# Performance work log

Measured on AMD Instinct MI355X. Metric: run time of the kernel, lower is better.

The kernel has to match this reference:

```python
import jax, jax.numpy as jnp
import numpy as np

B, C, OC, H, W = 2, 64, 128, 96, 96
HD, DI, N, R, K = C // 2, C, 16, 2, 4  # VSSBlock: hidden=C/2, d_inner=2*hidden=C, d_state, dt_rank, 4 scan dirs
EPS = 1e-5


def _conv(x, w, b, pad, groups=1):
    y = jax.lax.conv_general_dilated(x, w, (1, 1), pad, feature_group_count=groups,
                                     dimension_numbers=('NCHW', 'OIHW', 'NCHW'))
    return y + b[None, :, None, None]


def _ln(x, w, b):
    m = x.mean(-1, keepdims=True)
    v = x.var(-1, keepdims=True)
    return (x - m) * jax.lax.rsqrt(v + EPS) * w + b


def _selective_scan(xs, dts, Bs, Cs, A, D):
    # xs, dts: (B,K,DI,L); Bs, Cs: (B,K,N,L); A: (K,DI,N); D: (K,DI)
    dts = jax.nn.softplus(dts)

    def step(h, inp):
        u_t, dt_t, B_t, C_t = inp
        dA = jnp.exp(dt_t[..., None] * A)                         # (B,K,DI,N)
        h = dA * h + (dt_t * u_t)[..., None] * B_t[:, :, None, :]
        return h, jnp.einsum('bkdn,bkn->bkd', h, C_t)

    seq = (jnp.moveaxis(xs, -1, 0), jnp.moveaxis(dts, -1, 0),
           jnp.moveaxis(Bs, -1, 0), jnp.moveaxis(Cs, -1, 0))
    h0 = jnp.zeros(xs.shape[:3] + (A.shape[-1],), xs.dtype)
    _, ys = jax.lax.scan(step, h0, seq)
    return jnp.moveaxis(ys, 0, -1) + D[None, :, :, None] * xs


def _vss_block(x, ln_w, ln_b, in_w, conv_w, conv_b, xproj_w, dtproj_w, dtproj_b,
               A_logs, Ds, on_w, on_b, out_w):
    # x: (B,H,W,HD); VMamba SS2D with 4-direction cross-scan + residual
    b, hh, ww, _ = x.shape
    L = hh * ww
    h = _ln(x, ln_w, ln_b)
    xz = h @ in_w                                   # (B,H,W,2*DI)
    xp, z = jnp.split(xz, 2, axis=-1)
    xc = jnp.transpose(xp, (0, 3, 1, 2))            # (B,DI,H,W)
    xc = jax.nn.silu(_conv(xc, conv_w, conv_b, ((1, 1), (1, 1)), groups=DI))
    x_flat = xc.reshape(b, DI, L)
    x_wh = jnp.transpose(xc, (0, 1, 3, 2)).reshape(b, DI, L)
    x2 = jnp.stack([x_flat, x_wh], axis=1)
    xs = jnp.concatenate([x2, jnp.flip(x2, -1)], axis=1)      # (B,4,DI,L)
    x_dbl = jnp.einsum('bkdl,kcd->bkcl', xs, xproj_w)
    dts, Bs, Cs = jnp.split(x_dbl, [R, R + N], axis=2)
    dts = jnp.einsum('bkrl,kdr->bkdl', dts, dtproj_w) + dtproj_b[None, :, :, None]
    A = -jnp.exp(A_logs)
    ys = _selective_scan(xs, dts, Bs, Cs, A, Ds)              # (B,4,DI,L)
    inv = jnp.flip(ys[:, 2:4], -1)
    unwh = lambda t: jnp.transpose(t.reshape(b, DI, ww, hh), (0, 1, 3, 2)).reshape(b, DI, L)
    y = ys[:, 0] + inv[:, 0] + unwh(ys[:, 1]) + unwh(inv[:, 1])
    y = jnp.transpose(y.reshape(b, DI, hh, ww), (0, 2, 3, 1))
    y = _ln(y, on_w, on_b) * jax.nn.silu(z)
    return x + y @ out_w


def _forward(x, ms_dw33_w, ms_dw33_b, ms_in_w, ms_in_b, ms_scale,
             vss_ln_w, vss_ln_b, vss_in_w, vss_conv_w, vss_conv_b, vss_xproj_w,
             vss_dtproj_w, vss_dtproj_b, vss_A_logs, vss_Ds, vss_on_w, vss_on_b, vss_out_w,
             ma_conv_w, ma_conv_b, adw_h_w, adw_h_b, adw_w_w, adw_w_b,
             pw_w, pw_b, bn_w, bn_b, bn_mean, bn_var):
    vss = (vss_ln_w, vss_ln_b, vss_in_w, vss_conv_w, vss_conv_b, vss_xproj_w,
           vss_dtproj_w, vss_dtproj_b, vss_A_logs, vss_Ds, vss_on_w, vss_on_b, vss_out_w)
    # --- MambaSplit (shared VSSBlock applied to both channel halves) ---
    xd = _conv(x, ms_dw33_w, ms_dw33_b, ((1, 1), (1, 1)), groups=C)
    x1, x2 = jnp.split(xd, 2, axis=1)

    def branch(xp):
        y = _vss_block(jnp.transpose(xp, (0, 2, 3, 1)), *vss)
        return ms_scale * xp + jnp.transpose(y, (0, 3, 1, 2))

    xm = jnp.concatenate([branch(x1), branch(x2)], axis=1)
    m = xm.mean((2, 3), keepdims=True)
    v = xm.var((2, 3), keepdims=True)
    xm = (xm - m) * jax.lax.rsqrt(v + EPS) * ms_in_w[None, :, None, None] + ms_in_b[None, :, None, None]
    xm = jax.nn.leaky_relu(xm, 0.01)
    # --- MaxAvg (global avg+max pool -> 3x3 conv on 1x1 map -> sigmoid gate) ---
    pooled = jnp.concatenate([x.mean((2, 3), keepdims=True), x.max((2, 3), keepdims=True)], axis=1)
    gate = jax.nn.sigmoid(_conv(pooled, ma_conv_w, ma_conv_b, ((1, 1), (1, 1))))
    xs_ = xm + gate * x
    # --- AxialDW ---
    xs_ = xs_ + _conv(xs_, adw_h_w, adw_h_b, ((1, 1), (0, 0)), groups=C) \
              + _conv(xs_, adw_w_w, adw_w_b, ((0, 0), (1, 1)), groups=C)
    # --- BN (eval) + ReLU, 1x1 conv, 2x2 maxpool ---
    skip = jax.nn.relu((xs_ - bn_mean[None, :, None, None]) * jax.lax.rsqrt(bn_var[None, :, None, None] + EPS)
                       * bn_w[None, :, None, None] + bn_b[None, :, None, None])
    out = _conv(skip, pw_w, pw_b, ((0, 0), (0, 0)))
    down = jax.lax.reduce_window(out, -jnp.inf, jax.lax.max, (1, 1, 2, 2), (1, 1, 2, 2), 'VALID')
    return down, skip


def setup_inputs() -> dict:
    key = jax.random.key(0)
    ks = jax.random.split(key, 16)
    r = lambda i, shape, s=0.02: jax.random.normal(ks[i], shape, jnp.float32) * s
    return {
        'x': jax.random.normal(ks[0], (B, C, H, W), jnp.float32),
        'ms_dw33_w': r(1, (C, 1, 3, 3), 0.1), 'ms_dw33_b': jnp.zeros(C),
        'ms_in_w': jnp.ones(C), 'ms_in_b': jnp.zeros(C),
        'ms_scale': jnp.ones((1,)),
        'vss_ln_w': jnp.ones(HD), 'vss_ln_b': jnp.zeros(HD),
        'vss_in_w': r(2, (HD, 2 * DI)),
        'vss_conv_w': r(3, (DI, 1, 3, 3), 0.1), 'vss_conv_b': jnp.zeros(DI),
        'vss_xproj_w': r(4, (K, R + 2 * N, DI)),
        'vss_dtproj_w': r(5, (K, DI, R), 0.1), 'vss_dtproj_b': r(6, (K, DI), 0.1),
        'vss_A_logs': jnp.tile(jnp.log(jnp.arange(1, N + 1, dtype=jnp.float32)), (K, DI, 1)),
        'vss_Ds': jnp.ones((K, DI)),
        'vss_on_w': jnp.ones(DI), 'vss_on_b': jnp.zeros(DI),
        'vss_out_w': r(7, (DI, HD)),
        'ma_conv_w': r(8, (C, 2 * C, 3, 3), 0.05), 'ma_conv_b': jnp.zeros(C),
        'adw_h_w': r(9, (C, 1, 3, 1), 0.1), 'adw_h_b': jnp.zeros(C),
        'adw_w_w': r(10, (C, 1, 1, 3), 0.1), 'adw_w_b': jnp.zeros(C),
        'pw_w': r(11, (OC, C, 1, 1)), 'pw_b': jnp.zeros(OC),
        'bn_w': jnp.ones(C), 'bn_b': jnp.zeros(C),
        'bn_mean': jnp.zeros(C), 'bn_var': jnp.ones(C),
    }


def reference(x, ms_dw33_w, ms_dw33_b, ms_in_w, ms_in_b, ms_scale,
              vss_ln_w, vss_ln_b, vss_in_w, vss_conv_w, vss_conv_b, vss_xproj_w,
              vss_dtproj_w, vss_dtproj_b, vss_A_logs, vss_Ds, vss_on_w, vss_on_b, vss_out_w,
              ma_conv_w, ma_conv_b, adw_h_w, adw_h_b, adw_w_w, adw_w_b,
              pw_w, pw_b, bn_w, bn_b, bn_mean, bn_var):
    return _forward(x, ms_dw33_w, ms_dw33_b, ms_in_w, ms_in_b, ms_scale,
                    vss_ln_w, vss_ln_b, vss_in_w, vss_conv_w, vss_conv_b, vss_xproj_w,
                    vss_dtproj_w, vss_dtproj_b, vss_A_logs, vss_Ds, vss_on_w, vss_on_b, vss_out_w,
                    ma_conv_w, ma_conv_b, adw_h_w, adw_h_b, adw_w_w, adw_w_b,
                    pw_w, pw_b, bn_w, bn_b, bn_mean, bn_var)
```

## Files before the change

kernel.cpp:

```cpp
#include <hip/hip_runtime.h>
#include <hip/hip_bf16.h>

typedef __hip_bfloat16 bf16;
#define DEV __device__ __forceinline__

constexpr int B_ = 2, C_ = 64, H_ = 96, W_ = 96, L_ = 9216;
constexpr int HD_ = 32, DI_ = 64, N_ = 16, K_ = 4, BB_ = 4;
constexpr int OC_ = 128;
constexpr int CH_ = 384, CL_ = 24;
constexpr int SEGN = 32, SEGC = 12;
constexpr int BROW = 20;
constexpr float EPSF = 1e-5f;
constexpr int DOWN_SZ = B_ * OC_ * 48 * 48;

typedef __attribute__((ext_vector_type(8))) short short8;
typedef __attribute__((ext_vector_type(4))) float f32x4;
typedef __attribute__((ext_vector_type(2))) float f32x2;

DEV float softplusf(float x) { return x > 15.f ? x : __logf(1.f + __expf(x)); }
DEV float b2f(bf16 v) { return __bfloat162float(v); }
DEV float lo16f(unsigned v) { return __uint_as_float(v << 16); }
DEV float hi16f(unsigned v) { return __uint_as_float(v & 0xffff0000u); }
DEV f32x2 pk2(unsigned w) { f32x2 r = {lo16f(w), hi16f(w)}; return r; }
DEV void unpk8(uint4 a, float* v) {
  v[0] = lo16f(a.x); v[1] = hi16f(a.x); v[2] = lo16f(a.y); v[3] = hi16f(a.y);
  v[4] = lo16f(a.z); v[5] = hi16f(a.z); v[6] = lo16f(a.w); v[7] = hi16f(a.w);
}
DEV void unpk(uint4 a, uint4 b, float* v) {
  unpk8(a, v); unpk8(b, v + 8);
}

__constant__ float kLogN[16] = {
  0.0f, 0.69314718f, 1.09861229f, 1.38629436f, 1.60943791f, 1.79175947f,
  1.94591015f, 2.07944154f, 2.19722458f, 2.30258509f, 2.39789527f,
  2.48490665f, 2.56494936f, 2.63905733f, 2.70805020f, 2.77258872f};

DEV void pow_tree2(float e1, f32x2* ep) {
  float e2 = e1 * e1;
  ep[0].x = e1; ep[0].y = e2;
  f32x2 b2v = {e2, e2};
  ep[1] = ep[0] * b2v;
  float e4 = ep[1].y;
  f32x2 b4v = {e4, e4};
  ep[2] = ep[0] * b4v;
  ep[3] = ep[1] * b4v;
  float e8 = ep[3].y;
  f32x2 b8v = {e8, e8};
  ep[4] = ep[0] * b8v;
  ep[5] = ep[1] * b8v;
  ep[6] = ep[2] * b8v;
  ep[7] = ep[3] * b8v;
}

__global__ __launch_bounds__(256, 4) void k_front(
    const float* __restrict__ x, const float* __restrict__ dw33w,
    const float* __restrict__ dw33b, const float* __restrict__ lnw,
    const float* __restrict__ lnb, const float* __restrict__ inw,
    const float* __restrict__ xpw, const float* __restrict__ alog,
    float* __restrict__ xd, bf16* __restrict__ xzAh, bf16* __restrict__ xzBh,
    bf16* __restrict__ wh, float* __restrict__ aux) {
  int bb = blockIdx.y, t = threadIdx.x;
  int b = bb & 1, co = (bb >> 1) * HD_;
  int idx0 = blockIdx.x * 32;
  if (bb == 0) {
    int i = blockIdx.x * 256 + t;
    if (i < 144 * 64) {
      int n = i >> 6;
      wh[i] = __float2bfloat16(n < 136 ? xpw[i] : 0.f);
    }
    if (blockIdx.x == 0) {
      int kd = t;
      const float* al = alog + kd * N_;
      float a0 = al[0];
      bool lin = true;
#pragma unroll
      for (int n = 1; n < N_; n++) lin = lin && (fabsf(al[n] - a0 - kLogN[n]) < 3e-5f);
      aux[kd] = -__expf(a0);
      aux[256 + kd] = lin ? 1.f : 0.f;
#pragma unroll
      for (int n = 0; n < N_; n++) aux[512 + kd * N_ + n] = -__expf(al[n]);
    }
  }
  __shared__ float xds[32 * 36];
  __shared__ float meanA[32], rstdA[32];
  for (int i = t; i < 1024; i += 256) {
    int cl = i >> 5, ii = i & 31;
    int sp = idx0 + ii, wi = sp % 96, hi = sp / 96;
    int cg = b * C_ + co + cl;
    float acc = dw33b[co + cl];
#pragma unroll
    for (int dy = -1; dy <= 1; dy++) {
      int hh = hi + dy; if (hh < 0 || hh >= H_) continue;
#pragma unroll
      for (int dx = -1; dx <= 1; dx++) {
        int ww = wi + dx; if (ww < 0 || ww >= W_) continue;
        acc = fmaf(x[(size_t)cg * L_ + sp + dy * 96 + dx],
                   dw33w[(co + cl) * 9 + (dy + 1) * 3 + (dx + 1)], acc);
      }
    }
    xds[cl * 36 + ii] = acc;
    xd[(size_t)cg * L_ + sp] = acc;
  }
  __syncthreads();
  if (t < 32) {
    float s = 0.f, sq = 0.f;
#pragma unroll
    for (int c = 0; c < 32; c++) { float v = xds[c * 36 + t]; s += v; sq = fmaf(v, v, sq); }
    float mean = s * (1.f / HD_);
    float var = sq * (1.f / HD_) - mean * mean;
    meanA[t] = mean; rstdA[t] = rsqrtf(var + EPSF);
  }
  __syncthreads();
  for (int i = t; i < 1024; i += 256) {
    int c = i >> 5, idx = i & 31;
    float v = xds[c * 36 + idx];
    xds[c * 36 + idx] = (v - meanA[idx]) * rstdA[idx] * lnw[c] + lnb[c];
  }
  __syncthreads();
  int oc = t & 127, g = t >> 7;
  float acc[16];
#pragma unroll
  for (int j = 0; j < 16; j++) acc[j] = 0.f;
  for (int c = 0; c < 32; c++) {
    float wv = inw[c * 128 + oc];
    const float4* row = reinterpret_cast<const float4*>(&xds[c * 36 + g * 16]);
#pragma unroll
    for (int j4 = 0; j4 < 4; j4++) {
      float4 xv = row[j4];
      acc[j4 * 4 + 0] = fmaf(xv.x, wv, acc[j4 * 4 + 0]);
      acc[j4 * 4 + 1] = fmaf(xv.y, wv, acc[j4 * 4 + 1]);
      acc[j4 * 4 + 2] = fmaf(xv.z, wv, acc[j4 * 4 + 2]);
      acc[j4 * 4 + 3] = fmaf(xv.w, wv, acc[j4 * 4 + 3]);
    }
  }
  int occ = oc & 63;
  if (oc < 64) {
#pragma unroll
    for (int j = 0; j < 16; j++)
      xzAh[(size_t)(bb * L_ + idx0 + g * 16 + j) * 64 + occ] = __float2bfloat16(acc[j]);
  } else {
#pragma unroll
    for (int j = 0; j < 16; j++)
      xzBh[(size_t)(bb * L_ + idx0 + g * 16 + j) * 64 + occ] = __float2bfloat16(acc[j]);
  }
}

__global__ void k_dwsilu(const bf16* __restrict__ xzAh, const float* __restrict__ cw,
                         const float* __restrict__ cb, bf16* __restrict__ xch,
                         bf16* __restrict__ xcht) {
  int t = blockIdx.x * 256 + threadIdx.x;
  int d = t & 63, idx = (t >> 6) % L_, bb = t / (L_ * DI_);
  int wi = idx % W_, hi = idx / W_;
  float acc = cb[d];
#pragma unroll
  for (int dy = -1; dy <= 1; dy++) {
    int hh = hi + dy; if (hh < 0 || hh >= H_) continue;
#pragma unroll
    for (int dx = -1; dx <= 1; dx++) {
      int ww = wi + dx; if (ww < 0 || ww >= W_) continue;
      acc = fmaf(b2f(xzAh[(size_t)(bb * L_ + hh * W_ + ww) * 64 + d]),
                 cw[d * 9 + (dy + 1) * 3 + (dx + 1)], acc);
    }
  }
  acc = acc / (1.f + __expf(-acc));
  bf16 v = __float2bfloat16(acc);
  xch[t] = v;
  int idx_t = wi * 96 + hi;
  xcht[((size_t)bb * L_ + idx_t) * DI_ + d] = v;
}

__global__ __launch_bounds__(256, 4) void k_xdbl_mfma(
    const bf16* __restrict__ xch, const bf16* __restrict__ wh,
    float* __restrict__ xdblB, float* __restrict__ xdblC) {
  int w = threadIdx.x >> 6, lane = threadIdx.x & 63;
  int bb = blockIdx.y;
  int mtile = blockIdx.x * 4 + w;
  int idx0 = mtile * 16;
  int m = lane & 15, quad = lane >> 4;
  const bf16* arow = xch + ((size_t)bb * L_ + idx0 + m) * 64 + quad * 8;
  short8 a0 = *reinterpret_cast<const short8*>(arow);
  short8 a1 = *reinterpret_cast<const short8*>(arow + 32);
  int ntb = blockIdx.z * 3;
#pragma unroll
  for (int it = 0; it < 3; it++) {
    int nt = ntb + it;
    int n = nt * 16 + m;
    const bf16* brow = wh + n * 64 + quad * 8;
    short8 b0 = *reinterpret_cast<const short8*>(brow);
    short8 b1 = *reinterpret_cast<const short8*>(brow + 32);
    f32x4 acc = {0.f, 0.f, 0.f, 0.f};
    acc = __builtin_amdgcn_mfma_f32_16x16x32_bf16(a0, b0, acc, 0, 0, 0);
    acc = __builtin_amdgcn_mfma_f32_16x16x32_bf16(a1, b1, acc, 0, 0, 0);
    if (n < 136) {
      int k4 = (n >= 102) ? 3 : (n >= 68) ? 2 : (n >= 34) ? 1 : 0;
      int c = n - k4 * 34;
#pragma unroll
      for (int i = 0; i < 4; i++) {
        int r = idx0 + quad * 4 + i;
        int hi2 = r / 96, wi2 = r - hi2 * 96;
        int tr = wi2 * 96 + hi2;
        int ls = (k4 == 0) ? r : (k4 == 1) ? tr : (k4 == 2) ? (L_ - 1 - r) : (L_ - 1 - tr);
        size_t row = (size_t)(bb * K_ + k4) * L_ + ls;
        if (c < 2)       xdblB[row * BROW + 16 + c] = acc[i];
        else if (c < 18) xdblB[row * BROW + (c - 2)] = acc[i];
        else             xdblC[row * 16 + (c - 18)] = acc[i];
      }
    }
  }
}

__global__ __launch_bounds__(256, 4) void k_scan1(
    const float* __restrict__ xdblB, const bf16* __restrict__ xch,
    const bf16* __restrict__ xcht, const float* __restrict__ dtw,
    const float* __restrict__ dtb, const float* __restrict__ aux,
    bf16* __restrict__ hbuf, float* __restrict__ ssum) {
  int w = threadIdx.x >> 6, d = threadIdx.x & 63;
  int bx = blockIdx.x;
  int chunk = bx * 4 + w, k = blockIdx.y, bb = blockIdx.z;
  const float* bB = xdblB + (size_t)(bb * K_ + k) * L_ * BROW;
  __shared__ __align__(16) float sB[96 * BROW];
  {
    const uint4* src = (const uint4*)(bB + (size_t)bx * 96 * BROW);
    uint4* dst = (uint4*)sB;
    for (int i = threadIdx.x; i < 480; i += 256) dst[i] = src[i];
  }
  __syncthreads();
  float w0 = dtw[(k * DI_ + d) * 2 + 0], w1 = dtw[(k * DI_ + d) * 2 + 1];
  float bia = dtb[k * DI_ + d];
  float A1 = aux[k * 64 + d];
  bool chain = (__ballot(aux[256 + k * 64 + d] > 0.5f) == ~0ull);
  const bf16* ub = ((k & 1) ? xcht : xch) + (size_t)bb * L_ * DI_;
  int ls0 = chunk * CL_;
  int uidx0 = (k & 2) ? (L_ - 1 - ls0) : ls0;
  int ustep = (k & 2) ? -1 : 1;
  float S = 0.f;
  size_t base = (size_t)((bb * K_ + k) * CH_ + chunk) * DI_ + d;
  if (chain) {
    float uv[CL_];
    const bf16* up = ub + (size_t)uidx0 * DI_ + d;
#pragma unroll
    for (int s = 0; s < CL_; s++) uv[s] = b2f(up[s * ustep * DI_]);
    f32x2 h2[8];
#pragma unroll
    for (int i = 0; i < 8; i++) { h2[i].x = 0.f; h2[i].y = 0.f; }
#pragma unroll
    for (int s = 0; s < CL_; s++) {
      const float* p = sB + (w * CL_ + s) * BROW;
      float dt = softplusf(fmaf(p[16], w0, fmaf(p[17], w1, bia)));
      S += dt;
      float du = dt * uv[s];
      f32x2 du2 = {du, du};
      f32x2 ep2[8];
      pow_tree2(__expf(dt * A1), ep2);
#pragma unroll
      for (int i = 0; i < 8; i++)
        h2[i] = ep2[i] * h2[i] + du2 * (*(const f32x2*)(p + 2 * i));
    }
#pragma unroll
    for (int i = 0; i < 8; i++) {
      hbuf[base * N_ + 2 * i]     = __float2bfloat16(h2[i].x);
      hbuf[base * N_ + 2 * i + 1] = __float2bfloat16(h2[i].y);
    }
  } else {
    float h[N_];
#pragma unroll
    for (int n = 0; n < N_; n++) h[n] = 0.f;
    float A[N_];
#pragma unroll
    for (int n = 0; n < N_; n++) A[n] = aux[512 + (k * 64 + d) * N_ + n];
    for (int s = 0; s < CL_; s++) {
      const float* p = sB + (w * CL_ + s) * BROW;
      float u = b2f(ub[(size_t)(uidx0 + s * ustep) * DI_ + d]);
      float dt = softplusf(fmaf(p[16], w0, fmaf(p[17], w1, bia)));
      S += dt;
      float du = dt * u;
#pragma unroll
      for (int n = 0; n < N_; n++) h[n] = fmaf(__expf(dt * A[n]), h[n], du * p[n]);
    }
#pragma unroll
    for (int n = 0; n < N_; n++) hbuf[base * N_ + n] = __float2bfloat16(h[n]);
  }
  ssum[base] = S;
}

__global__ __launch_bounds__(256, 4) void k_scan2a(
    const float* __restrict__ aux, const float* __restrict__ ssum,
    bf16* __restrict__ hbuf, float* __restrict__ cumS,
    float* __restrict__ segH, float* __restrict__ segS) {
  int t = blockIdx.x * 256 + threadIdx.x;
  int n = t & 15, d = (t >> 4) & 63, kk = (t >> 10) & 3, bb = (t >> 12) & 3, seg = t >> 14;
  float A = aux[512 + (kk * 64 + d) * N_ + n];
  size_t row = (size_t)(bb * K_ + kk) * CH_ * DI_ + d;
  float hp = 0.f, Sc = 0.f;
#pragma unroll 4
  for (int j = 0; j < SEGC; j++) {
    int c = seg * SEGC + j;
    size_t sb = row + (size_t)c * DI_;
    float S = ssum[sb];
    float hl = b2f(hbuf[sb * N_ + n]);
    hbuf[sb * N_ + n] = __float2bfloat16(hp);
    if (n == 0) cumS[sb] = Sc;
    hp = fmaf(__expf(A * S), hp, hl);
    Sc += S;
  }
  size_t sbase = (size_t)(bb * K_ + kk) * SEGN + seg;
  segH[(sbase * DI_ + d) * N_ + n] = hp;
  if (n == 0) segS[sbase * DI_ + d] = Sc;
}

__global__ void k_scan2b(const float* __restrict__ aux, float* __restrict__ segH,
                         const float* __restrict__ segS) {
  int t = blockIdx.x * 256 + threadIdx.x;
  int n = t & 15, d = (t >> 4) & 63, kk = (t >> 10) & 3, bb = t >> 12;
  float A = aux[512 + (kk * 64 + d) * N_ + n];
  float hp = 0.f;
  for (int seg = 0; seg < SEGN; seg++) {
    size_t sbase = (size_t)(bb * K_ + kk) * SEGN + seg;
    size_t si = (sbase * DI_ + d) * N_ + n;
    float H = segH[si];
    float E = __expf(A * segS[sbase * DI_ + d]);
    segH[si] = hp;
    hp = fmaf(E, hp, H);
  }
}

__global__ __launch_bounds__(256, 4) void k_scan3(
    const float* __restrict__ xdblB, const float* __restrict__ xdblC,
    const bf16* __restrict__ xch, const bf16* __restrict__ xcht,
    const float* __restrict__ dtw, const float* __restrict__ dtb,
    const float* __restrict__ Dsw, const float* __restrict__ aux,
    const bf16* __restrict__ hbuf, const float* __restrict__ cumS,
    const float* __restrict__ segH, bf16* __restrict__ ydir) {
  int w = threadIdx.x >> 6, d = threadIdx.x & 63;
  int bx = blockIdx.x;
  int chunk = bx * 4 + w, k = blockIdx.y, bb = blockIdx.z;
  const float* bB = xdblB + (size_t)(bb * K_ + k) * L_ * BROW;
  const float* bC = xdblC + (size_t)(bb * K_ + k) * L_ * 16;
  __shared__ __align__(16) float sB[96 * BROW];
  __shared__ __align__(16) float sC[96 * 16];
  {
    const uint4* srcB = (const uint4*)(bB + (size_t)bx * 96 * BROW);
    uint4* dstB = (uint4*)sB;
    for (int i = threadIdx.x; i < 480; i += 256) dstB[i] = srcB[i];
    const uint4* srcC = (const uint4*)(bC + (size_t)bx * 96 * 16);
    uint4* dstC = (uint4*)sC;
    for (int i = threadIdx.x; i < 384; i += 256) dstC[i] = srcC[i];
  }
  __syncthreads();
  float w0 = dtw[(k * DI_ + d) * 2 + 0], w1 = dtw[(k * DI_ + d) * 2 + 1];
  float bia = dtb[k * DI_ + d];
  float Dk = Dsw[k * DI_ + d];
  float A1 = aux[k * 64 + d];
  bool chain = (__ballot(aux[256 + k * 64 + d] > 0.5f) == ~0ull);
  size_t base = (size_t)((bb * K_ + k) * CH_ + chunk) * DI_ + d;
  int seg = chunk / SEGC;
  size_t sbase = (size_t)(bb * K_ + k) * SEGN + seg;
  float Sc = cumS[base];
  const bf16* ub = ((k & 1) ? xcht : xch) + (size_t)bb * L_ * DI_;
  bf16* yb = ydir + (size_t)(bb * K_ + k) * L_ * DI_;
  int ls0 = chunk * CL_;
  int uidx0 = (k & 2) ? (L_ - 1 - ls0) : ls0;
  int ustep = (k & 2) ? -1 : 1;
  const bf16* hb = hbuf + base * N_;
  const float* Hin = segH + (sbase * DI_ + d) * N_;
  if (chain) {
    float uv[CL_];
    const bf16* up = ub + (size_t)uidx0 * DI_ + d;
#pragma unroll
    for (int s = 0; s < CL_; s++) uv[s] = b2f(up[s * ustep * DI_]);
    f32x2 h2[8];
    {
      uint4 qh0 = *(const uint4*)hb, qh1 = *(const uint4*)(hb + 8);
      h2[0] = pk2(qh0.x); h2[1] = pk2(qh0.y); h2[2] = pk2(qh0.z); h2[3] = pk2(qh0.w);
      h2[4] = pk2(qh1.x); h2[5] = pk2(qh1.y); h2[6] = pk2(qh1.z); h2[7] = pk2(qh1.w);
      f32x2 ep2[8];
      pow_tree2(__expf(A1 * Sc), ep2);
#pragma unroll
      for (int i = 0; i < 8; i++)
        h2[i] = ep2[i] * (*(const f32x2*)(Hin + 2 * i)) + h2[i];
    }
#pragma unroll
    for (int s = 0; s < CL_; s++) {
      int lr = w * CL_ + s;
      const float* p = sB + lr * BROW;
      const float* pc = sC + lr * 16;
      float dt = softplusf(fmaf(p[16], w0, fmaf(p[17], w1, bia)));
      float du = dt * uv[s];
      f32x2 du2 = {du, du};
      f32x2 ep2[8];
      pow_tree2(__expf(dt * A1), ep2);
      f32x2 y2 = {0.f, 0.f};
#pragma unroll
      for (int i = 0; i < 8; i++) {
        h2[i] = ep2[i] * h2[i] + du2 * (*(const f32x2*)(p + 2 * i));
        y2 = h2[i] * (*(const f32x2*)(pc + 2 * i)) + y2;
      }
      float y = fmaf(Dk, uv[s], y2.x + y2.y);
      yb[(size_t)(ls0 + s) * DI_ + d] = __float2bfloat16(y);
    }
  } else {
    float h[N_];
    {
      uint4 qh0 = *(const uint4*)hb, qh1 = *(const uint4*)(hb + 8);
      unpk(qh0, qh1, h);
#pragma unroll
      for (int n = 0; n < N_; n++) {
        float A = aux[512 + (k * 64 + d) * N_ + n];
        h[n] = fmaf(__expf(A * Sc), Hin[n], h[n]);
      }
    }
    float A[N_];
#pragma unroll
    for (int n = 0; n < N_; n++) A[n] = aux[512 + (k * 64 + d) * N_ + n];
    for (int s = 0; s < CL_; s++) {
      int lr = w * CL_ + s;
      const float* p = sB + lr * BROW;
      const float* pc = sC + lr * 16;
      float u = b2f(ub[(size_t)(uidx0 + s * ustep) * DI_ + d]);
      float dt = softplusf(fmaf(p[16], w0, fmaf(p[17], w1, bia)));
      float du = dt * u;
      float y = 0.f;
#pragma unroll
      for (int n = 0; n < N_; n++) {
        h[n] = fmaf(__expf(dt * A[n]), h[n], du * p[n]);
        y = fmaf(h[n], pc[n], y);
      }
      y = fmaf(Dk, u, y);
      yb[(size_t)(ls0 + s) * DI_ + d] = __float2bfloat16(y);
    }
  }
}

__global__ void k_combine(const bf16* __restrict__ ydir, const bf16* __restrict__ xzBh,
                          const float* __restrict__ xd, const float* __restrict__ onw,
                          const float* __restrict__ onb, const float* __restrict__ outw,
                          const float* __restrict__ mssc, float* __restrict__ xm) {
  int w = threadIdx.x >> 6, d = threadIdx.x & 63;
  int idx = blockIdx.x * 4 + w, bb = blockIdx.y;
  int b = bb & 1, co = (bb >> 1) * HD_;
  int hii = idx / 96, wii = idx - hii * 96;
  int lt = wii * 96 + hii;
  const bf16* yd = ydir + (size_t)bb * K_ * L_ * DI_;
  float y = b2f(yd[((size_t)0 * L_ + idx) * DI_ + d])
          + b2f(yd[((size_t)1 * L_ + lt) * DI_ + d])
          + b2f(yd[((size_t)2 * L_ + (L_ - 1 - idx)) * DI_ + d])
          + b2f(yd[((size_t)3 * L_ + (L_ - 1 - lt)) * DI_ + d]);
  float s = y, sq = y * y;
#pragma unroll
  for (int m = 1; m < 64; m <<= 1) { s += __shfl_xor(s, m, 64); sq += __shfl_xor(sq, m, 64); }
  float mean = s * (1.f / DI_);
  float var = sq * (1.f / DI_) - mean * mean;
  float rstd = rsqrtf(var + EPSF);
  float yn = (y - mean) * rstd * onw[d] + onb[d];
  float z = b2f(xzBh[(size_t)(bb * L_ + idx) * 64 + d]);
  float g = yn * (z / (1.f + __expf(-z)));
  __shared__ float gs[4][DI_];
  gs[w][d] = g;
  __syncthreads();
  if (d < HD_) {
    float acc = 0.f;
#pragma unroll
    for (int dd = 0; dd < DI_; dd++) acc = fmaf(gs[w][dd], outw[dd * HD_ + d], acc);
    size_t xi = (size_t)(b * C_ + co + d) * L_ + idx;
    float xp = xd[xi];
    xm[xi] = mssc[0] * xp + xp + acc;
  }
}

__global__ __launch_bounds__(1024) void k_stats(
    const float* __restrict__ xm, const float* __restrict__ x,
    float* __restrict__ inm, float* __restrict__ inr,
    float* __restrict__ xmean, float* __restrict__ xmax) {
  int bc = blockIdx.x, t = threadIdx.x;
  const float* pm = xm + (size_t)bc * L_;
  const float* px = x + (size_t)bc * L_;
  float s = 0.f, sq = 0.f, xs = 0.f, mx = -1e30f;
  for (int i = t; i < L_; i += 1024) {
    float v = pm[i]; s += v; sq = fmaf(v, v, sq);
    float xv = px[i]; xs += xv; mx = fmaxf(mx, xv);
  }
  __shared__ float red[64];
#pragma unroll
  for (int m = 1; m < 64; m <<= 1) {
    s += __shfl_xor(s, m, 64); sq += __shfl_xor(sq, m, 64);
    xs += __shfl_xor(xs, m, 64); mx = fmaxf(mx, __shfl_xor(mx, m, 64));
  }
  int wid = t >> 6;
  if ((t & 63) == 0) { red[wid] = s; red[16 + wid] = sq; red[32 + wid] = xs; red[48 + wid] = mx; }
  __syncthreads();
  if (t == 0) {
    s = 0.f; sq = 0.f; xs = 0.f; mx = -1e30f;
#pragma unroll
    for (int i = 0; i < 16; i++) {
      s += red[i]; sq += red[16 + i]; xs += red[32 + i]; mx = fmaxf(mx, red[48 + i]);
    }
    float mean = s * (1.f / L_);
    float var = sq * (1.f / L_) - mean * mean;
    inm[bc] = mean;
    inr[bc] = rsqrtf(var + EPSF);
    xmean[bc] = xs * (1.f / L_);
    xmax[bc] = mx;
  }
}

__global__ void k_axbn(const float* __restrict__ xm, const float* __restrict__ x,
                       const float* __restrict__ inm, const float* __restrict__ inr,
                       const float* __restrict__ msw, const float* __restrict__ msb,
                       const float* __restrict__ xmean, const float* __restrict__ xmax,
                       const float* __restrict__ maw, const float* __restrict__ mab,
                       const float* __restrict__ hw, const float* __restrict__ hb,
                       const float* __restrict__ wwt, const float* __restrict__ wb,
                       const float* __restrict__ bnw, const float* __restrict__ bnb,
                       const float* __restrict__ bnm, const float* __restrict__ bnv,
                       float* __restrict__ skipo) {
  constexpr int NEL = B_ * C_ * L_;
  int t0 = blockIdx.x * 256;
  int t = t0 + threadIdx.x;
  int bc = t0 / L_, c = bc & 63, b = bc >> 6;
  __shared__ float gsh;
  __shared__ float sxs[448];
  if (threadIdx.x < 64) {
    int ic = threadIdx.x;
    float p = xmean[b * 64 + ic] * maw[(c * 128 + ic) * 9 + 4]
            + xmax[b * 64 + ic] * maw[(c * 128 + 64 + ic) * 9 + 4];
#pragma unroll
    for (int m = 1; m < 64; m <<= 1) p += __shfl_xor(p, m, 64);
    if (ic == 0) gsh = 1.f / (1.f + __expf(-(p + mab[c])));
  }
  __syncthreads();
  float gate = gsh, im = inm[bc], ir = inr[bc], mw = msw[c], mb = msb[c];
  for (int i = threadIdx.x; i < 448; i += 256) {
    int tt = t0 - 96 + i;
    tt = tt < 0 ? 0 : (tt >= NEL ? NEL - 1 : tt);
    float v = xm[tt];
    v = (v - im) * ir * mw + mb;
    v = v > 0.f ? v : 0.01f * v;
    sxs[i] = v + gate * x[tt];
  }
  __syncthreads();
  int li = 96 + threadIdx.x;
  int wi = t % W_, hi = (t / W_) % H_;
  float a = sxs[li];
  float hacc = hb[c];
#pragma unroll
  for (int dy = -1; dy <= 1; dy++) {
    int hh = hi + dy; if (hh < 0 || hh >= H_) continue;
    hacc = fmaf(sxs[li + dy * 96], hw[c * 3 + dy + 1], hacc);
  }
  float wacc = wb[c];
#pragma unroll
  for (int dx = -1; dx <= 1; dx++) {
    int ww = wi + dx; if (ww < 0 || ww >= W_) continue;
    wacc = fmaf(sxs[li + dx], wwt[c * 3 + dx + 1], wacc);
  }
  float v = a + hacc + wacc;
  float sv = (v - bnm[c]) * rsqrtf(bnv[c] + EPSF) * bnw[c] + bnb[c];
  skipo[t] = fmaxf(sv, 0.f);
}

__global__ void k_pwpool(const float* __restrict__ skipo, const float* __restrict__ pww,
                         const float* __restrict__ pwb, float* __restrict__ down) {
  int h2 = blockIdx.x, b = blockIdx.y, t = threadIdx.x;
  int oc0 = blockIdx.z * 32;
  __shared__ float sk[64 * 192];
  for (int i = t; i < 64 * 192; i += 256) {
    int c = i / 192, rw = i % 192, r = rw / 96, wcol = rw % 96;
    sk[i] = skipo[((size_t)(b * C_ + c) * H_ + (2 * h2 + r)) * W_ + wcol];
  }
  __syncthreads();
  for (int o = t; o < 32 * 48; o += 256) {
    int oc = oc0 + o / 48, w2 = o % 48;
    float s0 = 0.f, s1 = 0.f, s2 = 0.f, s3 = 0.f;
#pragma unroll 8
    for (int c = 0; c < 64; c++) {
      float wv = pww[oc * 64 + c];
      const float* sp = &sk[c * 192 + 2 * w2];
      s0 = fmaf(sp[0], wv, s0);
      s1 = fmaf(sp[1], wv, s1);
      s2 = fmaf(sp[96], wv, s2);
      s3 = fmaf(sp[97], wv, s3);
    }
    float v = fmaxf(fmaxf(s0, s1), fmaxf(s2, s3)) + pwb[oc];
    down[((size_t)(b * OC_ + oc) * 48 + h2) * 48 + w2] = v;
  }
}

extern "C" void kernel_launch(void* const* d_in, const int* in_sizes, int n_in,
                              void* d_out, int out_size, void* d_ws, size_t ws_size,
                              hipStream_t stream) {
  const float* x     = (const float*)d_in[0];
  const float* dw33w = (const float*)d_in[1];
  const float* dw33b = (const float*)d_in[2];
  const float* msw   = (const float*)d_in[3];
  const float* msb   = (const float*)d_in[4];
  const float* mssc  = (const float*)d_in[5];
  const float* lnw   = (const float*)d_in[6];
  const float* lnb   = (const float*)d_in[7];
  const float* inw   = (const float*)d_in[8];
  const float* cw    = (const float*)d_in[9];
  const float* cb    = (const float*)d_in[10];
  const float* xpw   = (const float*)d_in[11];
  const float* dtw   = (const float*)d_in[12];
  const float* dtb   = (const float*)d_in[13];
  const float* alog  = (const float*)d_in[14];
  const float* Dsw   = (const float*)d_in[15];
  const float* onw   = (const float*)d_in[16];
  const float* onb   = (const float*)d_in[17];
  const float* outw  = (const float*)d_in[18];
  const float* maw   = (const float*)d_in[19];
  const float* mab   = (const float*)d_in[20];
  const float* ahw   = (const float*)d_in[21];
  const float* ahb   = (const float*)d_in[22];
  const float* aww   = (const float*)d_in[23];
  const float* awb   = (const float*)d_in[24];
  const float* pww   = (const float*)d_in[25];
  const float* pwb   = (const float*)d_in[26];
  const float* bnw   = (const float*)d_in[27];
  const float* bnb   = (const float*)d_in[28];
  const float* bnm   = (const float*)d_in[29];
  const float* bnv   = (const float*)d_in[30];

  float* ws = (float*)d_ws;
  float* xd    = ws;
  float* hreg  = xd + 1179648;
  bf16*  hbuf  = (bf16*)hreg;
  bf16*  xzAh  = (bf16*)hreg;
  bf16*  xzBh  = (bf16*)(hreg + 1179648);
  float* xdblB = hreg + 1179648 + 1179648;
  float* xdblC = xdblB + 2949120;
  float* ssum  = xdblC + 2359296;
  bf16*  ydir  = (bf16*)(ssum + 393216);
  float* xmR   = ssum + 393216 + 4718592;
  bf16*  xch   = (bf16*)xmR;
  float* xm    = xmR;
  float* st    = xmR + 1179648;
  float* inm = st, *inr = st + 128, *xmean = st + 256, *xmaxv = st + 384;
  float* aux   = st + 512;
  bf16*  wh    = (bf16*)(aux + 4608);
  float* cumS  = aux + 4608 + 4608;
  float* segH  = cumS + 393216;
  float* segS  = segH + 524288;
  bf16*  xcht  = (bf16*)(segS + 32768);

  float* outp = (float*)d_out;
  float* down = outp;
  float* skipo = outp + DOWN_SZ;

  dim3 b256(256);
  int nEl = B_ * C_ * L_;

  k_front<<<dim3(L_ / 32, BB_), b256, 0, stream>>>(x, dw33w, dw33b, lnw, lnb, inw,
                                                   xpw, alog, xd, xzAh, xzBh, wh, aux);
  k_dwsilu<<<dim3(BB_ * L_ * DI_ / 256), b256, 0, stream>>>(xzAh, cw, cb, xch, xcht);
  k_xdbl_mfma<<<dim3(L_ / 64, BB_, 3), b256, 0, stream>>>(xch, wh, xdblB, xdblC);
  k_scan1<<<dim3(CH_ / 4, K_, BB_), b256, 0, stream>>>(xdblB, xch, xcht, dtw, dtb, aux, hbuf, ssum);
  k_scan2a<<<dim3(BB_ * K_ * SEGN * DI_ * N_ / 256), b256, 0, stream>>>(aux, ssum, hbuf, cumS, segH, segS);
  k_scan2b<<<dim3(BB_ * K_ * DI_ * N_ / 256), b256, 0, stream>>>(aux, segH, segS);
  k_scan3<<<dim3(CH_ / 4, K_, BB_), b256, 0, stream>>>(xdblB, xdblC, xch, xcht, dtw, dtb, Dsw,
                                                      aux, hbuf, cumS, segH, ydir);
  k_combine<<<dim3(L_ / 4, BB_), b256, 0, stream>>>(ydir, xzBh, xd, onw, onb, outw, mssc, xm);
  k_stats<<<dim3(B_ * C_), dim3(1024), 0, stream>>>(xm, x, inm, inr, xmean, xmaxv);
  k_axbn<<<dim3((nEl + 255) / 256), b256, 0, stream>>>(xm, x, inm, inr, msw, msb, xmean, xmaxv,
                                                      maw, mab, ahw, ahb, aww, awb,
                                                      bnw, bnb, bnm, bnv, skipo);
  k_pwpool<<<dim3(48, B_, 4), b256, 0, stream>>>(skipo, pww, pwb, down);
}
```

Before: 293.4 us.

## Fuse scan2a/scan2b into one kernel and vectorize shared-memory loads

Merges the two inter-chunk scan passes into a single kernel. Each block owns one (batch, direction, channel, state-half) and performs the cross-segment carry in shared memory, which removes one launch and the segS round trip. Loads of B, C and the dt projections in the scan kernels are widened to float4/float2 reads from shared memory. The hbuf stores become packed 16-byte writes, and the pointwise-pool inner loop uses float2 reads. The new thread mapping gives scan2 different global access coalescing (8 states per block across 32 segments), and the serial 32-step loop in 8 threads adds a small tail.

```diff
diff --git a/kernel.cpp b/kernel.cpp
--- a/kernel.cpp
+++ b/kernel.cpp
@@ -22,6 +22,14 @@
 DEV float lo16f(unsigned v) { return __uint_as_float(v << 16); }
 DEV float hi16f(unsigned v) { return __uint_as_float(v & 0xffff0000u); }
 DEV f32x2 pk2(unsigned w) { f32x2 r = {lo16f(w), hi16f(w)}; return r; }
+DEV f32x2 lo2(f32x4 q) { f32x2 r = {q.x, q.y}; return r; }
+DEV f32x2 hi2(f32x4 q) { f32x2 r = {q.z, q.w}; return r; }
+DEV unsigned pkbf(float a, float b) {
+  __hip_bfloat162 t;
+  t.x = __float2bfloat16(a);
+  t.y = __float2bfloat16(b);
+  return *reinterpret_cast<unsigned*>(&t);
+}
 DEV void unpk8(uint4 a, float* v) {
   v[0] = lo16f(a.x); v[1] = hi16f(a.x); v[2] = lo16f(a.y); v[3] = hi16f(a.y);
   v[4] = lo16f(a.z); v[5] = hi16f(a.z); v[6] = lo16f(a.w); v[7] = hi16f(a.w);
@@ -246,21 +254,33 @@
 #pragma unroll
     for (int s = 0; s < CL_; s++) {
       const float* p = sB + (w * CL_ + s) * BROW;
-      float dt = softplusf(fmaf(p[16], w0, fmaf(p[17], w1, bia)));
+      f32x4 q0 = *(const f32x4*)p;
+      f32x4 q1 = *(const f32x4*)(p + 4);
+      f32x4 q2 = *(const f32x4*)(p + 8);
+      f32x4 q3 = *(const f32x4*)(p + 12);
+      f32x2 tt = *(const f32x2*)(p + 16);
+      float dt = softplusf(fmaf(tt.x, w0, fmaf(tt.y, w1, bia)));
       S += dt;
       float du = dt * uv[s];
       f32x2 du2 = {du, du};
       f32x2 ep2[8];
       pow_tree2(__expf(dt * A1), ep2);
-#pragma unroll
-      for (int i = 0; i < 8; i++)
-        h2[i] = ep2[i] * h2[i] + du2 * (*(const f32x2*)(p + 2 * i));
-    }
-#pragma unroll
-    for (int i = 0; i < 8; i++) {
-      hbuf[base * N_ + 2 * i]     = __float2bfloat16(h2[i].x);
-      hbuf[base * N_ + 2 * i + 1] = __float2bfloat16(h2[i].y);
-    }
+      h2[0] = ep2[0] * h2[0] + du2 * lo2(q0);
+      h2[1] = ep2[1] * h2[1] + du2 * hi2(q0);
+      h2[2] = ep2[2] * h2[2] + du2 * lo2(q1);
+      h2[3] = ep2[3] * h2[3] + du2 * hi2(q1);
+      h2[4] = ep2[4] * h2[4] + du2 * lo2(q2);
+      h2[5] = ep2[5] * h2[5] + du2 * hi2(q2);
+      h2[6] = ep2[6] * h2[6] + du2 * lo2(q3);
+      h2[7] = ep2[7] * h2[7] + du2 * hi2(q3);
+    }
+    uint4 o0, o1;
+    o0.x = pkbf(h2[0].x, h2[0].y); o0.y = pkbf(h2[1].x, h2[1].y);
+    o0.z = pkbf(h2[2].x, h2[2].y); o0.w = pkbf(h2[3].x, h2[3].y);
+    o1.x = pkbf(h2[4].x, h2[4].y); o1.y = pkbf(h2[5].x, h2[5].y);
+    o1.z = pkbf(h2[6].x, h2[6].y); o1.w = pkbf(h2[7].x, h2[7].y);
+    *(uint4*)(hbuf + base * N_) = o0;
+    *(uint4*)(hbuf + base * N_ + 8) = o1;
   } else {
     float h[N_];
 #pragma unroll
@@ -283,12 +303,15 @@
   ssum[base] = S;
 }
 
-__global__ __launch_bounds__(256, 4) void k_scan2a(
+__global__ __launch_bounds__(256, 4) void k_scan2(
     const float* __restrict__ aux, const float* __restrict__ ssum,
     bf16* __restrict__ hbuf, float* __restrict__ cumS,
-    float* __restrict__ segH, float* __restrict__ segS) {
-  int t = blockIdx.x * 256 + threadIdx.x;
-  int n = t & 15, d = (t >> 4) & 63, kk = (t >> 10) & 3, bb = (t >> 12) & 3, seg = t >> 14;
+    float* __restrict__ segH) {
+  int tid = threadIdx.x;
+  int r = tid & 7, seg = tid >> 3;
+  int bi = blockIdx.x;
+  int oct = bi & 1, d = (bi >> 1) & 63, kk = (bi >> 7) & 3, bb = bi >> 9;
+  int n = oct * 8 + r;
   float A = aux[512 + (kk * 64 + d) * N_ + n];
   size_t row = (size_t)(bb * K_ + kk) * CH_ * DI_ + d;
   float hp = 0.f, Sc = 0.f;
@@ -303,25 +326,21 @@
     hp = fmaf(__expf(A * S), hp, hl);
     Sc += S;
   }
+  __shared__ float sH[SEGN][8], sE[SEGN][8];
+  sH[seg][r] = hp;
+  sE[seg][r] = __expf(A * Sc);
+  __syncthreads();
+  if (tid < 8) {
+    float h = 0.f;
+    for (int s2 = 0; s2 < SEGN; s2++) {
+      float Hs = sH[s2][tid];
+      sH[s2][tid] = h;
+      h = fmaf(sE[s2][tid], h, Hs);
+    }
+  }
+  __syncthreads();
   size_t sbase = (size_t)(bb * K_ + kk) * SEGN + seg;
-  segH[(sbase * DI_ + d) * N_ + n] = hp;
-  if (n == 0) segS[sbase * DI_ + d] = Sc;
-}
-
-__global__ void k_scan2b(const float* __restrict__ aux, float* __restrict__ segH,
-                         const float* __restrict__ segS) {
-  int t = blockIdx.x * 256 + threadIdx.x;
-  int n = t & 15, d = (t >> 4) & 63, kk = (t >> 10) & 3, bb = t >> 12;
-  float A = aux[512 + (kk * 64 + d) * N_ + n];
-  float hp = 0.f;
-  for (int seg = 0; seg < SEGN; seg++) {
-    size_t sbase = (size_t)(bb * K_ + kk) * SEGN + seg;
-    size_t si = (sbase * DI_ + d) * N_ + n;
-    float H = segH[si];
-    float E = __expf(A * segS[sbase * DI_ + d]);
-    segH[si] = hp;
-    hp = fmaf(E, hp, H);
-  }
+  segH[(sbase * DI_ + d) * N_ + n] = sH[seg][r];
 }
 
 __global__ __launch_bounds__(256, 4) void k_scan3(
@@ -384,17 +403,29 @@
       int lr = w * CL_ + s;
       const float* p = sB + lr * BROW;
       const float* pc = sC + lr * 16;
-      float dt = softplusf(fmaf(p[16], w0, fmaf(p[17], w1, bia)));
+      f32x4 q0 = *(const f32x4*)p;
+      f32x4 q1 = *(const f32x4*)(p + 4);
+      f32x4 q2 = *(const f32x4*)(p + 8);
+      f32x4 q3 = *(const f32x4*)(p + 12);
+      f32x2 tt = *(const f32x2*)(p + 16);
+      f32x4 c0 = *(const f32x4*)pc;
+      f32x4 c1 = *(const f32x4*)(pc + 4);
+      f32x4 c2 = *(const f32x4*)(pc + 8);
+      f32x4 c3 = *(const f32x4*)(pc + 12);
+      float dt = softplusf(fmaf(tt.x, w0, fmaf(tt.y, w1, bia)));
       float du = dt * uv[s];
       f32x2 du2 = {du, du};
       f32x2 ep2[8];
       pow_tree2(__expf(dt * A1), ep2);
       f32x2 y2 = {0.f, 0.f};
-#pragma unroll
-      for (int i = 0; i < 8; i++) {
-        h2[i] = ep2[i] * h2[i] + du2 * (*(const f32x2*)(p + 2 * i));
-        y2 = h2[i] * (*(const f32x2*)(pc + 2 * i)) + y2;
-      }
+      h2[0] = ep2[0] * h2[0] + du2 * lo2(q0);  y2 = h2[0] * lo2(c0) + y2;
+      h2[1] = ep2[1] * h2[1] + du2 * hi2(q0);  y2 = h2[1] * hi2(c0) + y2;
+      h2[2] = ep2[2] * h2[2] + du2 * lo2(q1);  y2 = h2[2] * lo2(c1) + y2;
+      h2[3] = ep2[3] * h2[3] + du2 * hi2(q1);  y2 = h2[3] * hi2(c1) + y2;
+      h2[4] = ep2[4] * h2[4] + du2 * lo2(q2);  y2 = h2[4] * lo2(c2) + y2;
+      h2[5] = ep2[5] * h2[5] + du2 * hi2(q2);  y2 = h2[5] * hi2(c2) + y2;
+      h2[6] = ep2[6] * h2[6] + du2 * lo2(q3);  y2 = h2[6] * lo2(c3) + y2;
+      h2[7] = ep2[7] * h2[7] + du2 * hi2(q3);  y2 = h2[7] * hi2(c3) + y2;
       float y = fmaf(Dk, uv[s], y2.x + y2.y);
       yb[(size_t)(ls0 + s) * DI_ + d] = __float2bfloat16(y);
     }
@@ -562,7 +593,7 @@
                          const float* __restrict__ pwb, float* __restrict__ down) {
   int h2 = blockIdx.x, b = blockIdx.y, t = threadIdx.x;
   int oc0 = blockIdx.z * 32;
-  __shared__ float sk[64 * 192];
+  __shared__ __align__(8) float sk[64 * 192];
   for (int i = t; i < 64 * 192; i += 256) {
     int c = i / 192, rw = i % 192, r = rw / 96, wcol = rw % 96;
     sk[i] = skipo[((size_t)(b * C_ + c) * H_ + (2 * h2 + r)) * W_ + wcol];
@@ -574,11 +605,13 @@
 #pragma unroll 8
     for (int c = 0; c < 64; c++) {
       float wv = pww[oc * 64 + c];
-      const float* sp = &sk[c * 192 + 2 * w2];
-      s0 = fmaf(sp[0], wv, s0);
-      s1 = fmaf(sp[1], wv, s1);
-      s2 = fmaf(sp[96], wv, s2);
-      s3 = fmaf(sp[97], wv, s3);
+      const float2* sp = (const float2*)&sk[c * 192 + 2 * w2];
+      float2 r0 = sp[0];
+      float2 r1 = sp[48];
+      s0 = fmaf(r0.x, wv, s0);
+      s1 = fmaf(r0.y, wv, s1);
+      s2 = fmaf(r1.x, wv, s2);
+      s3 = fmaf(r1.y, wv, s3);
     }
     float v = fmaxf(fmaxf(s0, s1), fmaxf(s2, s3)) + pwb[oc];
     down[((size_t)(b * OC_ + oc) * 48 + h2) * 48 + w2] = v;
@@ -639,8 +672,7 @@
   bf16*  wh    = (bf16*)(aux + 4608);
   float* cumS  = aux + 4608 + 4608;
   float* segH  = cumS + 393216;
-  float* segS  = segH + 524288;
-  bf16*  xcht  = (bf16*)(segS + 32768);
+  bf16*  xcht  = (bf16*)(segH + 524288 + 32768);
 
   float* outp = (float*)d_out;
   float* down = outp;
@@ -654,8 +686,7 @@
   k_dwsilu<<<dim3(BB_ * L_ * DI_ / 256), b256, 0, stream>>>(xzAh, cw, cb, xch, xcht);
   k_xdbl_mfma<<<dim3(L_ / 64, BB_, 3), b256, 0, stream>>>(xch, wh, xdblB, xdblC);
   k_scan1<<<dim3(CH_ / 4, K_, BB_), b256, 0, stream>>>(xdblB, xch, xcht, dtw, dtb, aux, hbuf, ssum);
-  k_scan2a<<<dim3(BB_ * K_ * SEGN * DI_ * N_ / 256), b256, 0, stream>>>(aux, ssum, hbuf, cumS, segH, segS);
-  k_scan2b<<<dim3(BB_ * K_ * DI_ * N_ / 256), b256, 0, stream>>>(aux, segH, segS);
+  k_scan2<<<dim3(BB_ * K_ * DI_ * 2), b256, 0, stream>>>(aux, ssum, hbuf, cumS, segH);
   k_scan3<<<dim3(CH_ / 4, K_, BB_), b256, 0, stream>>>(xdblB, xdblC, xch, xcht, dtw, dtb, Dsw,
                                                       aux, hbuf, cumS, segH, ydir);
   k_combine<<<dim3(L_ / 4, BB_), b256, 0, stream>>>(ydir, xzBh, xd, onw, onb, outw, mssc, xm);
```

Result: slower. 321.6 us (+9.6%).
